# Kernel tuning notes

Measured on AMD Instinct MI355X. Metric: run time of the kernel, lower is better.

## Reference

```python
import jax, jax.numpy as jnp
import numpy as np

B, C, H, W = 2048, 1, 128, 128
TARGET_H, TARGET_W = 70, 70
SAVE = 64
CUT = 64
CX, CY = 64.0, 64.0  # hardcoded mask center in the torch code


def setup_inputs() -> dict:
    key = jax.random.key(0)
    k1, k2 = jax.random.split(key)
    image = jax.random.uniform(k1, (B, C, H, W), dtype=jnp.float32)  # SAR magnitude in [0,1)
    azimuth = jax.random.uniform(k2, (B,), dtype=jnp.float32) * 360.0  # degrees
    alpha = jnp.ones((4,), dtype=jnp.float32)  # nn.Parameter init
    return {"image": image, "azimuth": azimuth, "alpha": alpha}


def _rotate_nearest(img, angle_deg):
    """torchvision TF.rotate(img, angle, NEAREST, expand=False, fill=0).
    img: (c,h,w). Positive angle = counter-clockwise.
    Inverse affine map (output -> input), nearest sampling, zero padding."""
    c, h, w = img.shape
    a = jnp.deg2rad(angle_deg)
    xc = jnp.arange(w, dtype=img.dtype) - (w - 1) / 2.0
    yc = jnp.arange(h, dtype=img.dtype) - (h - 1) / 2.0
    X, Y = jnp.meshgrid(xc, yc)  # (h,w)
    cos, sin = jnp.cos(a), jnp.sin(a)
    xin = cos * X + sin * Y
    yin = -sin * X + cos * Y
    col = jnp.floor(xin + (w - 1) / 2.0 + 0.5)
    row = jnp.floor(yin + (h - 1) / 2.0 + 0.5)
    valid = (col >= 0) & (col < w) & (row >= 0) & (row < h)
    col_i = jax.lax.stop_gradient(jnp.clip(col, 0, w - 1).astype(jnp.int32))
    row_i = jax.lax.stop_gradient(jnp.clip(row, 0, h - 1).astype(jnp.int32))
    return img[:, row_i, col_i] * valid[None, :, :].astype(img.dtype)


def reference(image, azimuth, alpha):
    b, c, h, w = image.shape
    # --- mask_making: axis-aligned box around hardcoded center, scaled by alpha ---
    x_up = jnp.round(CX + alpha[0] * TARGET_H / 2.0)
    x_down = jnp.round(CX - alpha[1] * TARGET_H / 2.0)
    y_up = jnp.round(CY + alpha[2] * TARGET_W / 2.0)
    y_down = jnp.round(CY - alpha[3] * TARGET_W / 2.0)
    rows = jnp.arange(h, dtype=image.dtype)[:, None]
    cols = jnp.arange(w, dtype=image.dtype)[None, :]
    box = ((rows >= x_down) & (rows < x_up) & (cols >= y_down) & (cols < y_up)).astype(image.dtype)
    box = jnp.broadcast_to(box[None], (c, h, w))
    # per-sample rotation by -azimuth (vectorized across batch)
    masks = jax.vmap(lambda ang: _rotate_nearest(box, -ang))(azimuth)  # (b,c,h,w)

    # --- target_separating ---
    xs, xe = h // 2 - SAVE // 2, h // 2 + SAVE // 2
    target = (image * masks)[:, :, xs:xe, xs:xe]
    target_scene = image * (masks == 0).astype(image.dtype)

    # --- TargetCut ---
    image_eq = jnp.where(image * 2.0 >= 1.0, jnp.ones((), image.dtype), image * 2.0)
    cs, ce = h // 2 - CUT // 2, h // 2 + CUT // 2
    target_cut = image_eq[:, :, cs:ce, cs:ce]

    target_raw = image
    return (target, target_cut, target_scene, target_raw)
```

## Files before the change

### kernel.cpp

```cpp
#include <hip/hip_runtime.h>
#include <math.h>


#define NB 2048

__global__ __launch_bounds__(256) void kd_rotmask_kernel(
    const float* __restrict__ image,
    const float* __restrict__ azim,
    const float* __restrict__ alpha,
    float* __restrict__ out)
{
    const int b   = blockIdx.y;
    const int tid = blockIdx.x * 256 + threadIdx.x;

    __shared__ float s_cs, s_sn, s_xd, s_xu, s_yd, s_yu;
    if (threadIdx.x == 0) {
        float a = __fmul_rn(-azim[b], 0.017453292519943295f);
        double ad = (double)a;
        s_cs = (float)cos(ad);
        s_sn = (float)sin(ad);
        s_xu = rintf(__fadd_rn(64.0f, __fmul_rn(alpha[0], 35.0f)));
        s_xd = rintf(__fsub_rn(64.0f, __fmul_rn(alpha[1], 35.0f)));
        s_yu = rintf(__fadd_rn(64.0f, __fmul_rn(alpha[2], 35.0f)));
        s_yd = rintf(__fsub_rn(64.0f, __fmul_rn(alpha[3], 35.0f)));
    }
    __syncthreads();
    const float cs = s_cs, sn = s_sn;
    const float xd = s_xd, xu = s_xu, yd = s_yd, yu = s_yu;

    const int row  = tid >> 5;
    const int c4   = tid & 31;
    const int col0 = c4 << 2;

    const float4* img4 = (const float4*)image + (size_t)b * 4096 + tid;
    const float4 v = *img4;
    const float px[4] = {v.x, v.y, v.z, v.w};

    const float Yf = (float)row - 63.5f;
    float tgt[4], scn[4];
    #pragma unroll
    for (int j = 0; j < 4; ++j) {
        const float Xf = (float)(col0 + j) - 63.5f;
        const float xin = __fadd_rn(__fmul_rn(cs, Xf), __fmul_rn(sn, Yf));
        const float yin = __fadd_rn(__fmul_rn(-sn, Xf), __fmul_rn(cs, Yf));
        const float colf = floorf(__fadd_rn(__fadd_rn(xin, 63.5f), 0.5f));
        const float rowf = floorf(__fadd_rn(__fadd_rn(yin, 63.5f), 0.5f));
        const bool valid = (colf >= 0.0f) && (colf < 128.0f) &&
                           (rowf >= 0.0f) && (rowf < 128.0f);
        const float rc = fminf(fmaxf(rowf, 0.0f), 127.0f);
        const float cc = fminf(fmaxf(colf, 0.0f), 127.0f);
        const bool m = valid && (rc >= xd) && (rc < xu) && (cc >= yd) && (cc < yu);
        tgt[j] = m ? px[j] : 0.0f;
        scn[j] = m ? 0.0f : px[j];
    }

    float4* out4 = (float4*)out;
    const size_t full_idx = (size_t)b * 4096 + tid;
    out4[4194304u + full_idx]  = make_float4(scn[0], scn[1], scn[2], scn[3]);
    out4[12582912u + full_idx] = v;

    if (row >= 32 && row < 96 && c4 >= 8 && c4 < 24) {
        const size_t ti = (size_t)b * 1024 + (size_t)(row - 32) * 16 + (c4 - 8);
        out4[ti] = make_float4(tgt[0], tgt[1], tgt[2], tgt[3]);
        float cut[4];
        #pragma unroll
        for (int j = 0; j < 4; ++j) {
            const float e = __fmul_rn(px[j], 2.0f);
            cut[j] = (e >= 1.0f) ? 1.0f : e;
        }
        out4[2097152u + ti] = make_float4(cut[0], cut[1], cut[2], cut[3]);
    }
}

extern "C" void kernel_launch(void* const* d_in, const int* in_sizes, int n_in,
                              void* d_out, int out_size, void* d_ws, size_t ws_size,
                              hipStream_t stream) {
    const float* image = (const float*)d_in[0];
    const float* azim  = (const float*)d_in[1];
    const float* alpha = (const float*)d_in[2];
    float* out = (float*)d_out;

    dim3 grid(16, NB);
    dim3 block(256);
    hipLaunchKernelGGL(kd_rotmask_kernel, grid, block, 0, stream,
                       image, azim, alpha, out);
}
```

Before: 414.5 us.

## Precompute per-sample trig in prep kernel and process full image per block

Moves the double-precision cos/sin of each azimuth into a separate small kernel that writes to workspace. The main kernel now uses one block per sample that loops over all 16 row groups, instead of 16 blocks per sample each redoing the trig and a shared-memory barrier. Per-column rotation products are hoisted out of the row loop. This removes the serialized double-precision trig and syncthreads from every block, at the cost of an extra kernel launch and fewer, longer blocks.

```diff
diff --git a/kernel.cpp b/kernel.cpp
--- a/kernel.cpp
+++ b/kernel.cpp
@@ -4,71 +4,91 @@
 
 #define NB 2048
 
-__global__ __launch_bounds__(256) void kd_rotmask_kernel(
-    const float* __restrict__ image,
-    const float* __restrict__ azim,
-    const float* __restrict__ alpha,
-    float* __restrict__ out)
-{
-    const int b   = blockIdx.y;
-    const int tid = blockIdx.x * 256 + threadIdx.x;
+__global__ __launch_bounds__(256) void kd_prep(const float* __restrict__ azim,
+                                               float* __restrict__ trig) {
+    const int b = blockIdx.x * 256 + threadIdx.x;
+    if (b < NB) {
+        const float a = __fmul_rn(-azim[b], 0.017453292519943295f);
+        const double ad = (double)a;
+        trig[2 * b]     = (float)cos(ad);
+        trig[2 * b + 1] = (float)sin(ad);
+    }
+}
 
-    __shared__ float s_cs, s_sn, s_xd, s_xu, s_yd, s_yu;
-    if (threadIdx.x == 0) {
-        float a = __fmul_rn(-azim[b], 0.017453292519943295f);
-        double ad = (double)a;
-        s_cs = (float)cos(ad);
-        s_sn = (float)sin(ad);
-        s_xu = rintf(__fadd_rn(64.0f, __fmul_rn(alpha[0], 35.0f)));
-        s_xd = rintf(__fsub_rn(64.0f, __fmul_rn(alpha[1], 35.0f)));
-        s_yu = rintf(__fadd_rn(64.0f, __fmul_rn(alpha[2], 35.0f)));
-        s_yd = rintf(__fsub_rn(64.0f, __fmul_rn(alpha[3], 35.0f)));
-    }
-    __syncthreads();
-    const float cs = s_cs, sn = s_sn;
-    const float xd = s_xd, xu = s_xu, yd = s_yd, yu = s_yu;
+__global__ __launch_bounds__(256) void kd_main(const float* __restrict__ image,
+                                               const float* __restrict__ alpha,
+                                               const float* __restrict__ trig,
+                                               float* __restrict__ out) {
+    const int b = blockIdx.x;
+    const int t = threadIdx.x;
+    const float cs = trig[2 * b];
+    const float sn = trig[2 * b + 1];
+    const float xu = rintf(__fadd_rn(64.0f, __fmul_rn(alpha[0], 35.0f)));
+    const float xd = rintf(__fsub_rn(64.0f, __fmul_rn(alpha[1], 35.0f)));
+    const float yu = rintf(__fadd_rn(64.0f, __fmul_rn(alpha[2], 35.0f)));
+    const float yd = rintf(__fsub_rn(64.0f, __fmul_rn(alpha[3], 35.0f)));
 
-    const int row  = tid >> 5;
-    const int c4   = tid & 31;
+    const int c4   = t & 31;
+    const int r0   = t >> 5;
     const int col0 = c4 << 2;
+    const bool incropcol = (c4 >= 8) && (c4 < 24);
 
-    const float4* img4 = (const float4*)image + (size_t)b * 4096 + tid;
-    const float4 v = *img4;
-    const float px[4] = {v.x, v.y, v.z, v.w};
-
-    const float Yf = (float)row - 63.5f;
-    float tgt[4], scn[4];
+    float csX[4], nsX[4];
     #pragma unroll
     for (int j = 0; j < 4; ++j) {
         const float Xf = (float)(col0 + j) - 63.5f;
-        const float xin = __fadd_rn(__fmul_rn(cs, Xf), __fmul_rn(sn, Yf));
-        const float yin = __fadd_rn(__fmul_rn(-sn, Xf), __fmul_rn(cs, Yf));
-        const float colf = floorf(__fadd_rn(__fadd_rn(xin, 63.5f), 0.5f));
-        const float rowf = floorf(__fadd_rn(__fadd_rn(yin, 63.5f), 0.5f));
-        const bool valid = (colf >= 0.0f) && (colf < 128.0f) &&
-                           (rowf >= 0.0f) && (rowf < 128.0f);
-        const float rc = fminf(fmaxf(rowf, 0.0f), 127.0f);
-        const float cc = fminf(fmaxf(colf, 0.0f), 127.0f);
-        const bool m = valid && (rc >= xd) && (rc < xu) && (cc >= yd) && (cc < yu);
-        tgt[j] = m ? px[j] : 0.0f;
-        scn[j] = m ? 0.0f : px[j];
+        csX[j] = __fmul_rn(cs, Xf);
+        nsX[j] = __fmul_rn(-sn, Xf);
     }
 
-    float4* out4 = (float4*)out;
-    const size_t full_idx = (size_t)b * 4096 + tid;
-    out4[4194304u + full_idx]  = make_float4(scn[0], scn[1], scn[2], scn[3]);
-    out4[12582912u + full_idx] = v;
+    const float4* __restrict__ img4 = (const float4*)image + (size_t)b * 4096;
+    float4* __restrict__ out4 = (float4*)out;
+    const size_t fullbase = (size_t)b * 4096;
 
-    if (row >= 32 && row < 96 && c4 >= 8 && c4 < 24) {
-        const size_t ti = (size_t)b * 1024 + (size_t)(row - 32) * 16 + (c4 - 8);
-        out4[ti] = make_float4(tgt[0], tgt[1], tgt[2], tgt[3]);
-        float cut[4];
+    #pragma unroll
+    for (int i = 0; i < 16; ++i) {
+        const int row = r0 + (i << 3);
+        const int k   = (row << 5) + c4;
+        const float4 v = img4[k];
+        const float px[4] = {v.x, v.y, v.z, v.w};
+
+        const float Yf  = (float)row - 63.5f;
+        const float snY = __fmul_rn(sn, Yf);
+        const float csY = __fmul_rn(cs, Yf);
+
+        float tgt[4], scn[4];
         #pragma unroll
         for (int j = 0; j < 4; ++j) {
-            const float e = __fmul_rn(px[j], 2.0f);
-            cut[j] = (e >= 1.0f) ? 1.0f : e;
+            const float xin  = __fadd_rn(csX[j], snY);
+            const float yin  = __fadd_rn(nsX[j], csY);
+            const float colf = floorf(__fadd_rn(__fadd_rn(xin, 63.5f), 0.5f));
+            const float rowf = floorf(__fadd_rn(__fadd_rn(yin, 63.5f), 0.5f));
+            const bool valid = (colf >= 0.0f) && (colf < 128.0f) &&
+                               (rowf >= 0.0f) && (rowf < 128.0f);
+            const float rc = fminf(fmaxf(rowf, 0.0f), 127.0f);
+            const float cc = fminf(fmaxf(colf, 0.0f), 127.0f);
+            const bool m = valid && (rc >= xd) && (rc < xu) &&
+                           (cc >= yd) && (cc < yu);
+            tgt[j] = m ? px[j] : 0.0f;
+            scn[j] = m ? 0.0f : px[j];
         }
-        out4[2097152u + ti] = make_float4(cut[0], cut[1], cut[2], cut[3]);
+
+        out4[4194304u + fullbase + k]  =
+            make_float4(scn[0], scn[1], scn[2], scn[3]);
+        out4[12582912u + fullbase + k] = v;
+
+        if (i >= 4 && i < 12 && incropcol) {
+            const size_t ti = (size_t)b * 1024 + (size_t)(row - 32) * 16
+                              + (size_t)(c4 - 8);
+            out4[ti] = make_float4(tgt[0], tgt[1], tgt[2], tgt[3]);
+            float cut[4];
+            #pragma unroll
+            for (int j = 0; j < 4; ++j) {
+                const float e = __fmul_rn(px[j], 2.0f);
+                cut[j] = (e >= 1.0f) ? 1.0f : e;
+            }
+            out4[2097152u + ti] = make_float4(cut[0], cut[1], cut[2], cut[3]);
+        }
     }
 }
 
@@ -78,10 +98,10 @@
     const float* image = (const float*)d_in[0];
     const float* azim  = (const float*)d_in[1];
     const float* alpha = (const float*)d_in[2];
-    float* out = (float*)d_out;
+    float* out  = (float*)d_out;
+    float* trig = (float*)d_ws;
 
-    dim3 grid(16, NB);
-    dim3 block(256);
-    hipLaunchKernelGGL(kd_rotmask_kernel, grid, block, 0, stream,
-                       image, azim, alpha, out);
+    hipLaunchKernelGGL(kd_prep, dim3(NB / 256), dim3(256), 0, stream, azim, trig);
+    hipLaunchKernelGGL(kd_main, dim3(NB), dim3(256), 0, stream,
+                       image, alpha, trig, out);
 }
```

After: 431.7 us. 1.04x slower.
